# Performance work log

Measured on AMD Instinct MI355X. Metric: run time of the kernel, lower is better.

The kernel has to match this reference:

```python
import jax, jax.numpy as jnp
import numpy as np

B, N, K, NUM_CLASSES = 8, 4096, 20, 40


def _knn_idx(x, k):
    # x: [B, N, D] -> indices of k nearest neighbors (self excluded), [B, N, k]
    sq = jnp.sum(x * x, axis=-1)  # [B, N]
    dist = sq[:, :, None] + sq[:, None, :] - 2.0 * jnp.einsum('bnd,bmd->bnm', x, x)
    dist = jnp.where(jnp.eye(x.shape[1], dtype=bool)[None], jnp.inf, dist)
    return jax.lax.top_k(-dist, k)[1]


def _edge_conv(x, idx, params):
    # PyG EdgeConv with max aggregation: max_j MLP([x_i, x_j - x_i])
    x_j = jax.vmap(lambda xb, ib: xb[ib])(x, idx)              # [B, N, K, D]
    x_i = jnp.broadcast_to(x[:, :, None, :], x_j.shape)        # [B, N, K, D]
    h = jnp.concatenate([x_i, x_j - x_i], axis=-1)             # [B, N, K, 2D]
    for w, b in params:
        h = jax.nn.relu(h @ w + b)
    return jnp.max(h, axis=2)                                  # [B, N, out]


def setup_inputs() -> dict:
    key = jax.random.key(0)
    ks = jax.random.split(key, 12)

    def lin(k, i, o):  # torch Linear default init
        k1, k2 = jax.random.split(k)
        s = 1.0 / np.sqrt(i)
        return (jax.random.uniform(k1, (i, o), jnp.float32, -s, s),
                jax.random.uniform(k2, (o,), jnp.float32, -s, s))

    inp = {
        'pos': jax.random.normal(ks[0], (B * N, 3), jnp.float32),
        'batch': jnp.repeat(jnp.arange(B, dtype=jnp.int32), N),
    }
    names = [('m1w1', 'm1b1', 6, 64), ('m1w2', 'm1b2', 64, 64), ('m1w3', 'm1b3', 64, 64),
             ('m2w1', 'm2b1', 128, 128), ('m2w2', 'm2b2', 128, 128), ('m2w3', 'm2b3', 128, 256),
             ('lin0_w', 'lin0_b', 256, 512), ('lin1_w', 'lin1_b', 512, 256),
             ('lin2_w', 'lin2_b', 256, 256), ('lin3_w', 'lin3_b', 256, NUM_CLASSES)]
    for t, (wn, bn, i, o) in enumerate(names):
        w, b = lin(ks[t + 1], i, o)
        inp[wn] = w
        inp[bn] = b
    return inp


def reference(pos, batch, m1w1, m1b1, m1w2, m1b2, m1w3, m1b3,
              m2w1, m2b1, m2w2, m2b2, m2w3, m2b3,
              lin0_w, lin0_b, lin1_w, lin1_b, lin2_w, lin2_b, lin3_w, lin3_b):
    x = pos.reshape(B, N, 3)
    x = _edge_conv(x, _knn_idx(x, K), [(m1w1, m1b1), (m1w2, m1b2), (m1w3, m1b3)])   # [B,N,64]
    x = _edge_conv(x, _knn_idx(x, K), [(m2w1, m2b1), (m2w2, m2b2), (m2w3, m2b3)])   # [B,N,256]
    x = jax.nn.relu(x @ lin0_w + lin0_b)                                            # [B,N,512]
    x = jax.ops.segment_max(x.reshape(B * N, -1), batch, num_segments=B)            # [B,512]
    x = jax.nn.relu(x @ lin1_w + lin1_b)
    x = jax.nn.relu(x @ lin2_w + lin2_b)   # dropout is identity in eval mode
    x = x @ lin3_w + lin3_b
    return jax.nn.log_softmax(x, axis=-1)
```

## Files before the change

### kernel.cpp

```cpp
#include <hip/hip_runtime.h>

#define DEVI static __device__ __forceinline__

typedef __attribute__((ext_vector_type(4))) float f32x4;
typedef __attribute__((ext_vector_type(8))) short short8;
typedef __attribute__((ext_vector_type(4))) short short4v;
typedef __attribute__((ext_vector_type(8))) __bf16 bf16x8;

#define N_    4096
#define KNN_  20
#define NPTS  32768

DEVI unsigned short f2bf(float f){
  unsigned u = __float_as_uint(f);
  u += 0x7FFFu + ((u >> 16) & 1u);
  return (unsigned short)(u >> 16);
}
DEVI float bf2f(unsigned short s){ return __uint_as_float(((unsigned)s) << 16); }
DEVI float bf2fs(short s){ return __uint_as_float(((unsigned)(unsigned short)s) << 16); }
DEVI unsigned umin32(unsigned a, unsigned b){ return a < b ? a : b; }
DEVI unsigned umax32(unsigned a, unsigned b){ return a > b ? a : b; }

DEVI f32x4 mfma16(short8 a, short8 b, f32x4 c){
  return __builtin_amdgcn_mfma_f32_16x16x32_bf16(
      __builtin_bit_cast(bf16x8, a), __builtin_bit_cast(bf16x8, b), c, 0, 0, 0);
}

DEVI short8 lds_frag(const unsigned short* buf, int row, int k0, int strideS, int swzMask){
  return *(const short8*)(buf + row*strideS + (k0 ^ ((row & swzMask) << 3)));
}
DEVI void lds_put8(unsigned short* buf, int row, int k0, int strideS, int swzMask, short8 v){
  *(short8*)(buf + row*strideS + (k0 ^ ((row & swzMask) << 3))) = v;
}

DEVI void ins32(unsigned K, unsigned (&a)[20]){
#pragma unroll
  for (int t = 19; t >= 1; --t) a[t] = umin32(a[t], umax32(a[t-1], K));
  a[0] = umin32(a[0], K);
}
DEVI void ins64(double K, double (&a)[20]){
#pragma unroll
  for (int t = 19; t >= 1; --t) a[t] = fmin(a[t], fmax(a[t-1], K));
  a[0] = fmin(a[0], K);
}

__global__ __launch_bounds__(256) void p3_k(const float* __restrict__ pos,
    unsigned short* __restrict__ p3h, unsigned short* __restrict__ p3l, float* __restrict__ nrm3){
  int p = blockIdx.x*256 + threadIdx.x;
  if (p >= NPTS) return;
  float x = pos[(size_t)p*3], y = pos[(size_t)p*3+1], z = pos[(size_t)p*3+2];
  float v[8] = {x, y, z, 0.f, 0.f, 0.f, 0.f, 0.f};
#pragma unroll
  for (int c = 0; c < 8; ++c){
    unsigned short h = f2bf(v[c]);
    p3h[(size_t)p*8 + c] = h;
    p3l[(size_t)p*8 + c] = f2bf(v[c] - bf2f(h));
  }
  nrm3[p] = fmaf(x, x, fmaf(y, y, z*z));
}

template<int MODE>
__global__ __launch_bounds__(256) void knn_k(const unsigned short* __restrict__ Xh,
                                             const unsigned short* __restrict__ Xl,
                                             const float* __restrict__ nrm,
                                             unsigned* __restrict__ pk){
  constexpr int BSTR = MODE ? 4096 : 512;
  constexpr int OBL  = MODE ? 16384 : 2048;
  constexpr int OBUF = MODE ? 32768 : 4096;
  constexpr int OTHR = OBUF + 6144;
  constexpr int OSQ  = OTHR + 256;
  constexpr int SM   = MODE ? (OSQ + 512) : 15360;
  __shared__ __align__(16) char smem[SM];
  unsigned short* BhA = (unsigned short*)(smem);
  unsigned short* BlA = (unsigned short*)(smem + OBL);
  unsigned* buf      = (unsigned*)(smem + OBUF);
  unsigned* rowThr   = (unsigned*)(smem + OTHR);
  float* sqjA        = (float*)(smem + OSQ);
  unsigned* mD       = (unsigned*)(smem);

  const int blk = blockIdx.x;
  const int rt = blk & 63, ch = (blk >> 6) & 1, bb = blk >> 7;
  const int rowbase = rt * 64, cbase = ch * 2048;
  const size_t gb = (size_t)bb * N_;
  const int tid = threadIdx.x, lane = tid & 63, wid = tid >> 6;
  const int l15 = lane & 15, g = lane >> 4, kL = g << 3, r0 = g << 2;
  const int qidx = wid*16 + l15;

  if (tid < 64) rowThr[tid] = 0xFFFFFFFFu;

  short8 qh0 = {0,0,0,0,0,0,0,0}, qh1 = {0,0,0,0,0,0,0,0};
  short8 ql0 = {0,0,0,0,0,0,0,0}, ql1 = {0,0,0,0,0,0,0,0};
  if (MODE == 1){
    const size_t ab = (gb + rowbase + qidx) * 64;
    qh0 = *(const short8*)(Xh + ab + kL);
    qh1 = *(const short8*)(Xh + ab + 32 + kL);
    ql0 = *(const short8*)(Xl + ab + kL);
    ql1 = *(const short8*)(Xl + ab + 32 + kL);
  } else {
    if (g == 0){
      const size_t ab = (gb + rowbase + qidx) * 8;
      qh0 = *(const short8*)(Xh + ab);
      ql0 = *(const short8*)(Xl + ab);
    }
  }
  const float si = nrm[gb + rowbase + qidx];

  unsigned arr[20];
#pragma unroll
  for (int t = 0; t < 20; ++t) arr[t] = 0xFFFFFFFFu;
  int cnt = 0;
  bool selfR[4];
#pragma unroll
  for (int r = 0; r < 4; ++r) selfR[r] = (l15 == r0 + r);

  if (MODE == 1){
    for (int f = tid; f < 512; f += 256){
      int lf = f & 63, half = (f >> 6) & 1, ct = f >> 7;
      int row = ct*16 + (lf & 15);
      int col = half*32 + ((lf >> 4) << 3);
      const size_t src = (gb + cbase + row) * 64 + col;
      *(short8*)(BhA + f*8) = *(const short8*)(Xh + src);
      *(short8*)(BlA + f*8) = *(const short8*)(Xl + src);
    }
  } else {
    if (tid < 64)       *(short8*)(BhA + tid*8)      = *(const short8*)(Xh + (gb + cbase + tid)*8);
    else if (tid < 128) *(short8*)(BlA + (tid-64)*8) = *(const short8*)(Xl + (gb + cbase + (tid-64))*8);
  }
  if (tid < 64) sqjA[tid] = nrm[gb + cbase + tid];
  __syncthreads();

  for (int c = 0; c < 32; ++c){
    const int cur = c & 1;
    const unsigned short* Bh = BhA + cur*BSTR;
    const unsigned short* Bl = BlA + cur*BSTR;
    const float* sqj = sqjA + cur*64;
    const bool selfTile = (cbase + c*64 == rowbase);
    const bool more = (c + 1 < 32);

    short8 nh0 = {0,0,0,0,0,0,0,0}, nh1 = {0,0,0,0,0,0,0,0};
    short8 nl0 = {0,0,0,0,0,0,0,0}, nl1 = {0,0,0,0,0,0,0,0};
    float nsq = 0.f;
    if (more){
      if (MODE == 1){
#pragma unroll
        for (int ff = 0; ff < 2; ++ff){
          int f = tid + ff*256;
          int lf = f & 63, half = (f >> 6) & 1, ct = f >> 7;
          int row = ct*16 + (lf & 15);
          int col = half*32 + ((lf >> 4) << 3);
          const size_t src = (gb + cbase + (c+1)*64 + row) * 64 + col;
          if (ff == 0){ nh0 = *(const short8*)(Xh + src); nl0 = *(const short8*)(Xl + src); }
          else        { nh1 = *(const short8*)(Xh + src); nl1 = *(const short8*)(Xl + src); }
        }
      } else {
        if (tid < 64)       nh0 = *(const short8*)(Xh + (gb + cbase + (c+1)*64 + tid)*8);
        else if (tid < 128) nl0 = *(const short8*)(Xl + (gb + cbase + (c+1)*64 + (tid-64))*8);
      }
      if (tid < 64) nsq = nrm[gb + cbase + (c+1)*64 + tid];
    }

    unsigned kb16[16];
#pragma unroll
    for (int ct = 0; ct < 4; ++ct){
      f32x4 acc = {0.f,0.f,0.f,0.f};
      if (MODE == 1){
        const int fb = lane*8;
        short8 ch0 = *(const short8*)(Bh + (ct*2+0)*512 + fb);
        short8 ch1 = *(const short8*)(Bh + (ct*2+1)*512 + fb);
        short8 cl0 = *(const short8*)(Bl + (ct*2+0)*512 + fb);
        short8 cl1 = *(const short8*)(Bl + (ct*2+1)*512 + fb);
        acc = mfma16(ch0, qh0, acc); acc = mfma16(ch1, qh1, acc);
        acc = mfma16(cl0, qh0, acc); acc = mfma16(cl1, qh1, acc);
        acc = mfma16(ch0, ql0, acc); acc = mfma16(ch1, ql1, acc);
      } else {
        short8 cb = {0,0,0,0,0,0,0,0}, cl_ = {0,0,0,0,0,0,0,0};
        if (g == 0){
          cb  = *(const short8*)(Bh + (ct*16 + l15)*8);
          cl_ = *(const short8*)(Bl + (ct*16 + l15)*8);
        }
        acc = mfma16(cb,  qh0, acc);
        acc = mfma16(cl_, qh0, acc);
        acc = mfma16(cb,  ql0, acc);
      }
      f32x4 sj4 = *(const f32x4*)(sqj + ct*16 + r0);
#pragma unroll
      for (int r = 0; r < 4; ++r){
        unsigned cid = (unsigned)(c*64 + ct*16 + r0 + r);
        float dv = fmaxf(fmaf(-2.f, acc[r], si + sj4[r]), 0.f);
        unsigned kb = (__float_as_uint(dv) & ~0x7FFu) | cid;
        if (selfTile && ct == wid && selfR[r]) kb = 0x7F800000u | cid;
        kb16[ct*4 + r] = kb;
      }
    }

    {
      unsigned thrP = rowThr[qidx];
#pragma unroll
      for (int i = 0; i < 16; ++i){
        unsigned kb = kb16[i];
        if (kb < thrP){
          if (cnt < 6){ buf[cnt*256 + tid] = kb; ++cnt; }
          else ins32(kb, arr);
        }
      }
      for (int t = 0; t < cnt; ++t) ins32(buf[t*256 + tid], arr);
      cnt = 0;
      atomicMin(&rowThr[qidx], arr[19]);
    }

    if (more){
      unsigned short* BhN = BhA + (cur^1)*BSTR;
      unsigned short* BlN = BlA + (cur^1)*BSTR;
      if (MODE == 1){
        *(short8*)(BhN + tid*8)       = nh0;
        *(short8*)(BhN + (tid+256)*8) = nh1;
        *(short8*)(BlN + tid*8)       = nl0;
        *(short8*)(BlN + (tid+256)*8) = nl1;
      } else {
        if (tid < 64)       *(short8*)(BhN + tid*8)      = nh0;
        else if (tid < 128) *(short8*)(BlN + (tid-64)*8) = nl0;
      }
      if (tid < 64) sqjA[(cur^1)*64 + tid] = nsq;
    }
    __syncthreads();
  }
  __syncthreads();
  if (g > 0){
#pragma unroll
    for (int t = 0; t < 20; ++t) mD[(qidx*3 + g-1)*20 + t] = arr[t];
  }
  __syncthreads();
  if (g == 0){
    for (int gg = 0; gg < 3; ++gg)
#pragma unroll
      for (int t = 0; t < 20; ++t) ins32(mD[(qidx*3 + gg)*20 + t], arr);
    const size_t gp = gb + rowbase + qidx;
#pragma unroll
    for (int t = 0; t < 20; ++t) pk[((size_t)(ch*20 + t))*NPTS + gp] = arr[t];
  }
}

__global__ __launch_bounds__(256) void knn_merge_k(const unsigned* __restrict__ pk,
                                                   int* __restrict__ idx){
  const int p = blockIdx.x*256 + threadIdx.x;
  double arr[20];
#pragma unroll
  for (int t = 0; t < 20; ++t){
    unsigned k = pk[(size_t)t*NPTS + p];
    unsigned long long K = (((unsigned long long)(k & ~0x7FFu)) << 1) | (k & 0x7FFu);
    arr[t] = __builtin_bit_cast(double, K);
  }
#pragma unroll
  for (int t = 0; t < 20; ++t){
    unsigned k = pk[(size_t)(20 + t)*NPTS + p];
    unsigned long long K = (((unsigned long long)(k & ~0x7FFu)) << 1) | (2048u + (k & 0x7FFu));
    ins64(__builtin_bit_cast(double, K), arr);
  }
  int* o = idx + (size_t)p*KNN_;
#pragma unroll
  for (int t = 0; t < 20; ++t)
    o[t] = (int)(__builtin_bit_cast(unsigned long long, arr[t]) & 0xFFFu);
}

__global__ void stage_w_k(const float* __restrict__ src, unsigned short* __restrict__ dh,
                          unsigned short* __restrict__ dl, int K, int Nw, int KT, int NT){
  int tid = blockIdx.x*256 + threadIdx.x;
  if (tid >= NT*KT*64) return;
  int l = tid & 63;
  int kk = (tid >> 6) % KT;
  int nt = tid / (64*KT);
  int n = nt*16 + (l & 15);
  int kb = kk*32 + ((l >> 4) << 3);
#pragma unroll
  for (int e=0;e<8;++e){
    int k = kb + e;
    float w = (k < K) ? src[(size_t)k*Nw + n] : 0.f;
    unsigned short h = f2bf(w);
    dh[(size_t)tid*8 + e] = h;
    if (dl) dl[(size_t)tid*8 + e] = f2bf(w - bf2f(h));
  }
}

__global__ __launch_bounds__(256) void ec1_k(const float* __restrict__ pos, const int* __restrict__ idx1,
    const unsigned short* __restrict__ W1h, const unsigned short* __restrict__ W1l,
    const unsigned short* __restrict__ W2h, const unsigned short* __restrict__ W2l,
    const unsigned short* __restrict__ W3h, const unsigned short* __restrict__ W3l,
    const float* __restrict__ b1, const float* __restrict__ b2, const float* __restrict__ b3,
    unsigned short* __restrict__ x1h, unsigned short* __restrict__ x1l, float* __restrict__ nrm1){
  __shared__ __align__(16) char smem[51200];
  unsigned short* Ah  = (unsigned short*)(smem);
  unsigned short* Al  = (unsigned short*)(smem + 5120);
  unsigned short* H1h = (unsigned short*)(smem + 10240);
  unsigned short* H1l = (unsigned short*)(smem + 20480);
  unsigned short* H2h = (unsigned short*)(smem + 30720);
  unsigned short* H2l = (unsigned short*)(smem + 40960);
  float* dump = (float*)(smem);
  const int p0 = blockIdx.x * 4;
  const int bb = p0 >> 12;
  const int tid = threadIdx.x, lane = tid & 63, wid = tid >> 6;
  const int l15 = lane & 15, g = lane >> 4, r0 = g << 2;

  if (tid < 80){
    int p = p0 + tid/20, slot = tid%20;
    int j = idx1[(size_t)p*KNN_ + slot];
    int gj = (bb << 12) + j;
    float a6[6];
    a6[0] = pos[(size_t)p*3]; a6[1] = pos[(size_t)p*3+1]; a6[2] = pos[(size_t)p*3+2];
    a6[3] = pos[(size_t)gj*3]   - a6[0];
    a6[4] = pos[(size_t)gj*3+1] - a6[1];
    a6[5] = pos[(size_t)gj*3+2] - a6[2];
    int mt = tid >> 4, lrow = tid & 15;
    short8 vh, vl, zz = {0,0,0,0,0,0,0,0};
#pragma unroll
    for (int c=0;c<8;++c){
      float v = (c < 6) ? a6[c] : 0.f;
      unsigned short h = f2bf(v);
      vh[c] = (short)h;
      vl[c] = (short)f2bf(v - bf2f(h));
    }
    *(short8*)(Ah + (mt*64 + lrow)*8) = vh;
    *(short8*)(Al + (mt*64 + lrow)*8) = vl;
#pragma unroll
    for (int gg=1;gg<4;++gg){
      *(short8*)(Ah + (mt*64 + gg*16 + lrow)*8) = zz;
      *(short8*)(Al + (mt*64 + gg*16 + lrow)*8) = zz;
    }
  }
  __syncthreads();
  const int nt = wid;
  const int kk2 = nt >> 1, sub2 = (nt & 1)*2 + (g >> 1), e0 = (g & 1)*4;
  {
    short8 wh = *(const short8*)(W1h + ((size_t)nt*64 + lane)*8);
    short8 wl = *(const short8*)(W1l + ((size_t)nt*64 + lane)*8);
    f32x4 b4 = *(const f32x4*)(b1 + nt*16 + r0);
    for (int mt=0; mt<5; ++mt){
      short8 ah = *(const short8*)(Ah + (mt*64 + lane)*8);
      short8 al = *(const short8*)(Al + (mt*64 + lane)*8);
      f32x4 acc = {0.f,0.f,0.f,0.f};
      acc = mfma16(wh, ah, acc);
      acc = mfma16(wl, ah, acc);
      acc = mfma16(wh, al, acc);
      short4v vh4, vl4;
#pragma unroll
      for (int r=0;r<4;++r){
        float v = fmaxf(acc[r] + b4[r], 0.f);
        unsigned short h = f2bf(v);
        vh4[r] = (short)h;
        vl4[r] = (short)f2bf(v - bf2f(h));
      }
      *(short4v*)(H1h + ((mt*2 + kk2)*64 + sub2*16 + l15)*8 + e0) = vh4;
      *(short4v*)(H1l + ((mt*2 + kk2)*64 + sub2*16 + l15)*8 + e0) = vl4;
    }
  }
  __syncthreads();
  {
    short8 wh0 = *(const short8*)(W2h + ((size_t)(nt*2+0)*64 + lane)*8);
    short8 wh1 = *(const short8*)(W2h + ((size_t)(nt*2+1)*64 + lane)*8);
    short8 wl0 = *(const short8*)(W2l + ((size_t)(nt*2+0)*64 + lane)*8);
    short8 wl1 = *(const short8*)(W2l + ((size_t)(nt*2+1)*64 + lane)*8);
    f32x4 b4 = *(const f32x4*)(b2 + nt*16 + r0);
    for (int mt=0; mt<5; ++mt){
      short8 ah0 = *(const short8*)(H1h + ((mt*2+0)*64 + lane)*8);
      short8 ah1 = *(const short8*)(H1h + ((mt*2+1)*64 + lane)*8);
      short8 al0 = *(const short8*)(H1l + ((mt*2+0)*64 + lane)*8);
      short8 al1 = *(const short8*)(H1l + ((mt*2+1)*64 + lane)*8);
      f32x4 acc = {0.f,0.f,0.f,0.f};
      acc = mfma16(wh0, ah0, acc); acc = mfma16(wh1, ah1, acc);
      acc = mfma16(wl0, ah0, acc); acc = mfma16(wl1, ah1, acc);
      acc = mfma16(wh0, al0, acc); acc = mfma16(wh1, al1, acc);
      short4v vh4, vl4;
#pragma unroll
      for (int r=0;r<4;++r){
        float v = fmaxf(acc[r] + b4[r], 0.f);
        unsigned short h = f2bf(v);
        vh4[r] = (short)h;
        vl4[r] = (short)f2bf(v - bf2f(h));
      }
      *(short4v*)(H2h + ((mt*2 + kk2)*64 + sub2*16 + l15)*8 + e0) = vh4;
      *(short4v*)(H2l + ((mt*2 + kk2)*64 + sub2*16 + l15)*8 + e0) = vl4;
    }
  }
  __syncthreads();
  {
    short8 wh0 = *(const short8*)(W3h + ((size_t)(nt*2+0)*64 + lane)*8);
    short8 wh1 = *(const short8*)(W3h + ((size_t)(nt*2+1)*64 + lane)*8);
    short8 wl0 = *(const short8*)(W3l + ((size_t)(nt*2+0)*64 + lane)*8);
    short8 wl1 = *(const short8*)(W3l + ((size_t)(nt*2+1)*64 + lane)*8);
    f32x4 b4 = *(const f32x4*)(b3 + nt*16 + r0);
    for (int mt=0; mt<5; ++mt){
      short8 ah0 = *(const short8*)(H2h + ((mt*2+0)*64 + lane)*8);
      short8 ah1 = *(const short8*)(H2h + ((mt*2+1)*64 + lane)*8);
      short8 al0 = *(const short8*)(H2l + ((mt*2+0)*64 + lane)*8);
      short8 al1 = *(const short8*)(H2l + ((mt*2+1)*64 + lane)*8);
      f32x4 acc = {0.f,0.f,0.f,0.f};
      acc = mfma16(wh0, ah0, acc); acc = mfma16(wh1, ah1, acc);
      acc = mfma16(wl0, ah0, acc); acc = mfma16(wl1, ah1, acc);
      acc = mfma16(wh0, al0, acc); acc = mfma16(wh1, al1, acc);
      f32x4 o;
#pragma unroll
      for (int r=0;r<4;++r) o[r] = fmaxf(acc[r] + b4[r], 0.f);
      int edge = mt*16 + l15;
      *(f32x4*)(dump + edge*68 + nt*16 + r0) = o;
    }
  }
  __syncthreads();
  if (tid < 64){
    int p = tid >> 4, c4 = tid & 15;
    int st = tid % 20;
    float mx[4] = {0.f,0.f,0.f,0.f};
    for (int e=0;e<20;++e){
      int ee = st + e; if (ee >= 20) ee -= 20;
      f32x4 v = *(const f32x4*)(dump + (p*20 + ee)*68 + c4*4);
#pragma unroll
      for (int r=0;r<4;++r) mx[r] = fmaxf(mx[r], v[r]);
    }
    int gp = p0 + p;
    short4v h4, l4;
    float s = 0.f;
#pragma unroll
    for (int r=0;r<4;++r){
      float m = mx[r];
      unsigned short h = f2bf(m);
      h4[r] = (short)h;
      l4[r] = (short)f2bf(m - bf2f(h));
      s = fmaf(m, m, s);
    }
    *(short4v*)(x1h + (size_t)gp*64 + c4*4) = h4;
    *(short4v*)(x1l + (size_t)gp*64 + c4*4) = l4;
    s += __shfl_xor(s, 1); s += __shfl_xor(s, 2); s += __shfl_xor(s, 4); s += __shfl_xor(s, 8);
    if (c4 == 0) nrm1[gp] = s;
  }
}

__global__ __launch_bounds__(256) void ec2_k(const unsigned short* __restrict__ x1h, const int* __restrict__ idx2,
    const unsigned short* __restrict__ V1, const unsigned short* __restrict__ V2, const unsigned short* __restrict__ V3,
    const float* __restrict__ b1, const float* __restrict__ b2, const float* __restrict__ b3,
    unsigned short* __restrict__ x2b){
  __shared__ __align__(16) char smem[81920];
  unsigned short* A  = (unsigned short*)(smem);
  unsigned short* H1 = (unsigned short*)(smem + 40960);
  const int p0 = blockIdx.x * 8, bb = p0 >> 12;
  const int tid = threadIdx.x, lane = tid & 63, wid = tid >> 6;
  const int l15 = lane & 15, r0 = (lane >> 4) << 2;

  if (tid < 160){
    int p = p0 + tid/20, slot = tid%20;
    int j = idx2[(size_t)p*KNN_ + slot];
    int gj = (bb << 12) + j;
    const unsigned short* xi = x1h + (size_t)p*64;
    const unsigned short* xj = x1h + (size_t)gj*64;
    int mt = tid >> 4, lrow = tid & 15;
#pragma unroll
    for (int q=0;q<8;++q){
      short8 vi = *(const short8*)(xi + q*8);
      short8 vj = *(const short8*)(xj + q*8);
      short8 vd;
#pragma unroll
      for (int c=0;c<8;++c) vd[c] = (short)f2bf(bf2fs(vj[c]) - bf2fs(vi[c]));
      *(short8*)(A + (((mt*4 + (q>>2))*64) + (q&3)*16 + lrow)*8) = vi;
      *(short8*)(A + (((mt*4 + 2 + (q>>2))*64) + (q&3)*16 + lrow)*8) = vd;
    }
  }
  __syncthreads();

  {
    short8 w[2][4];
#pragma unroll
    for (int ni=0;ni<2;++ni)
#pragma unroll
      for (int kk=0;kk<4;++kk)
        w[ni][kk] = *(const short8*)(V1 + ((size_t)((wid*2+ni)*4+kk)*64 + lane)*8);
    f32x4 b4[2];
    b4[0] = *(const f32x4*)(b1 + (wid*2+0)*16 + r0);
    b4[1] = *(const f32x4*)(b1 + (wid*2+1)*16 + r0);
    for (int mt=0; mt<10; ++mt){
      short8 bfr[4];
#pragma unroll
      for (int kk=0;kk<4;++kk) bfr[kk] = *(const short8*)(A + ((mt*4+kk)*64 + lane)*8);
#pragma unroll
      for (int ni=0;ni<2;++ni){
        int nt = wid*2 + ni;
        f32x4 acc = {0.f,0.f,0.f,0.f};
#pragma unroll
        for (int kk=0;kk<4;++kk) acc = mfma16(w[ni][kk], bfr[kk], acc);
        short4v v4;
#pragma unroll
        for (int r=0;r<4;++r) v4[r] = (short)f2bf(fmaxf(acc[r] + b4[ni][r], 0.f));
        int kk2 = nt >> 1, sub2 = (nt & 1)*2 + (r0 >> 3);
        *(short4v*)(H1 + ((mt*4+kk2)*64 + sub2*16 + l15)*8 + (r0 & 4)) = v4;
      }
    }
  }
  __syncthreads();
  {
    short8 w[2][4];
#pragma unroll
    for (int ni=0;ni<2;++ni)
#pragma unroll
      for (int kk=0;kk<4;++kk)
        w[ni][kk] = *(const short8*)(V2 + ((size_t)((wid*2+ni)*4+kk)*64 + lane)*8);
    f32x4 b4[2];
    b4[0] = *(const f32x4*)(b2 + (wid*2+0)*16 + r0);
    b4[1] = *(const f32x4*)(b2 + (wid*2+1)*16 + r0);
    for (int mt=0; mt<10; ++mt){
      short8 bfr[4];
#pragma unroll
      for (int kk=0;kk<4;++kk) bfr[kk] = *(const short8*)(H1 + ((mt*4+kk)*64 + lane)*8);
#pragma unroll
      for (int ni=0;ni<2;++ni){
        int nt = wid*2 + ni;
        f32x4 acc = {0.f,0.f,0.f,0.f};
#pragma unroll
        for (int kk=0;kk<4;++kk) acc = mfma16(w[ni][kk], bfr[kk], acc);
        short4v v4;
#pragma unroll
        for (int r=0;r<4;++r) v4[r] = (short)f2bf(fmaxf(acc[r] + b4[ni][r], 0.f));
        int kk2 = nt >> 1, sub2 = (nt & 1)*2 + (r0 >> 3);
        *(short4v*)(A + ((mt*4+kk2)*64 + sub2*16 + l15)*8 + (r0 & 4)) = v4;
      }
    }
  }
  __syncthreads();
  for (int g2=0; g2<2; ++g2){
    {
      short8 w[2][4];
#pragma unroll
      for (int ni=0;ni<2;++ni)
#pragma unroll
        for (int kk=0;kk<4;++kk)
          w[ni][kk] = *(const short8*)(V3 + ((size_t)((g2*8 + wid*2+ni)*4+kk)*64 + lane)*8);
      f32x4 b4[2];
      b4[0] = *(const f32x4*)(b3 + (g2*8 + wid*2+0)*16 + r0);
      b4[1] = *(const f32x4*)(b3 + (g2*8 + wid*2+1)*16 + r0);
      for (int mt=0; mt<10; ++mt){
        short8 bfr[4];
#pragma unroll
        for (int kk=0;kk<4;++kk) bfr[kk] = *(const short8*)(A + ((mt*4+kk)*64 + lane)*8);
#pragma unroll
        for (int ni=0;ni<2;++ni){
          int ntl = wid*2 + ni;
          f32x4 acc = {0.f,0.f,0.f,0.f};
#pragma unroll
          for (int kk=0;kk<4;++kk) acc = mfma16(w[ni][kk], bfr[kk], acc);
          short4v v4;
#pragma unroll
          for (int r=0;r<4;++r) v4[r] = (short)f2bf(fmaxf(acc[r] + b4[ni][r], 0.f));
          int kk2 = ntl >> 1, sub2 = (ntl & 1)*2 + (r0 >> 3);
          *(short4v*)(H1 + ((mt*4+kk2)*64 + sub2*16 + l15)*8 + (r0 & 4)) = v4;
        }
      }
    }
    __syncthreads();
    if (tid < 128){
      int p = tid >> 4, c8 = tid & 15;
      int kk = c8 >> 2, sub = c8 & 3;
      unsigned short mx[8];
#pragma unroll
      for (int e=0;e<8;++e) mx[e] = 0;
      for (int e=0;e<20;++e){
        int ee = e + p + c8; ee -= (ee >= 20) ? 20 : 0; ee -= (ee >= 20) ? 20 : 0;
        int row = p*20 + ee;
        short8 v = *(const short8*)(H1 + (((row>>4)*4 + kk)*64 + sub*16 + (row & 15))*8);
#pragma unroll
        for (int k2=0;k2<8;++k2){
          unsigned short u = (unsigned short)v[k2];
          mx[k2] = u > mx[k2] ? u : mx[k2];
        }
      }
      short8 o;
#pragma unroll
      for (int k2=0;k2<8;++k2) o[k2] = (short)mx[k2];
      *(short8*)(x2b + (size_t)(p0 + p)*256 + g2*128 + c8*8) = o;
    }
    __syncthreads();
  }
}

__global__ __launch_bounds__(256) void lin0_k(const unsigned short* __restrict__ x2b, const unsigned short* __restrict__ W0s,
                                              const float* __restrict__ b0, unsigned* __restrict__ pool){
  __shared__ __align__(16) char smem[67584];
  unsigned short* A = (unsigned short*)(smem);
  unsigned* ploc = (unsigned*)(smem + 65536);
  const int blk = blockIdx.x; const size_t row0 = (size_t)blk * 128; const int bb = blk >> 5;
  const int tid = threadIdx.x, lane = tid & 63, wid = tid >> 6;
  for (int it = tid; it < 4096; it += 256){
    int row = it >> 5, q = (it & 31) << 3;
    lds_put8(A, row, q, 256, 7, *(const short8*)(x2b + (row0 + row)*256 + q));
  }
  ploc[tid] = 0u; ploc[tid+256] = 0u;
  __syncthreads();
  const int l15 = lane & 15, kL = (lane >> 4) << 3;
  short8 af[2][8];
#pragma unroll
  for (int m=0;m<2;++m)
#pragma unroll
    for (int kk=0;kk<8;++kk)
      af[m][kk] = lds_frag(A, (wid*2+m)*16 + l15, kk*32 + kL, 256, 7);
  for (int nt=0; nt<32; ++nt){
    f32x4 a0 = {0.f,0.f,0.f,0.f}, a1 = {0.f,0.f,0.f,0.f};
#pragma unroll
    for (int kk=0;kk<8;++kk){
      short8 w = *(const short8*)(W0s + ((size_t)(nt*8+kk)*64 + lane)*8);
      a0 = mfma16(af[0][kk], w, a0);
      a1 = mfma16(af[1][kk], w, a1);
    }
    int col = nt*16 + l15;
    float m = fmaxf(fmaxf(fmaxf(a0[0],a0[1]),fmaxf(a0[2],a0[3])),
                    fmaxf(fmaxf(a1[0],a1[1]),fmaxf(a1[2],a1[3])));
    m = fmaxf(m + b0[col], 0.f);
    atomicMax(&ploc[col], __float_as_uint(m));
  }
  __syncthreads();
  atomicMax(&pool[(size_t)bb*512 + tid], ploc[tid]);
  atomicMax(&pool[(size_t)bb*512 + tid + 256], ploc[tid+256]);
}

__global__ __launch_bounds__(256) void head_k(const unsigned* __restrict__ pool,
    const float* __restrict__ w1, const float* __restrict__ bb1,
    const float* __restrict__ w2, const float* __restrict__ bb2,
    const float* __restrict__ w3, const float* __restrict__ bb3,
    float* __restrict__ out){
  __shared__ float pl[8*512];
  __shared__ float y1[8*256];
  __shared__ float y2[8*256];
  __shared__ float lg[8*40];
  const int tid = threadIdx.x;
  for (int it = tid; it < 4096; it += 256) pl[it] = __uint_as_float(pool[it]);
  __syncthreads();
  {
    float acc[8]; float bv = bb1[tid];
#pragma unroll
    for (int r=0;r<8;++r) acc[r] = bv;
    for (int k=0;k<512;++k){
      float w = w1[(size_t)k*256 + tid];
#pragma unroll
      for (int r=0;r<8;++r) acc[r] = fmaf(pl[r*512+k], w, acc[r]);
    }
#pragma unroll
    for (int r=0;r<8;++r) y1[r*256+tid] = fmaxf(acc[r], 0.f);
  }
  __syncthreads();
  {
    float acc[8]; float bv = bb2[tid];
#pragma unroll
    for (int r=0;r<8;++r) acc[r] = bv;
    for (int k=0;k<256;++k){
      float w = w2[(size_t)k*256 + tid];
#pragma unroll
      for (int r=0;r<8;++r) acc[r] = fmaf(y1[r*256+k], w, acc[r]);
    }
#pragma unroll
    for (int r=0;r<8;++r) y2[r*256+tid] = fmaxf(acc[r], 0.f);
  }
  __syncthreads();
  if (tid < 40){
    float acc[8]; float bv = bb3[tid];
#pragma unroll
    for (int r=0;r<8;++r) acc[r] = bv;
    for (int k=0;k<256;++k){
      float w = w3[(size_t)k*40 + tid];
#pragma unroll
      for (int r=0;r<8;++r) acc[r] = fmaf(y2[r*256+k], w, acc[r]);
    }
#pragma unroll
    for (int r=0;r<8;++r) lg[r*40+tid] = acc[r];
  }
  __syncthreads();
  if (tid < 8){
    float m = -__builtin_inff();
    for (int c2=0;c2<40;++c2) m = fmaxf(m, lg[tid*40+c2]);
    float s = 0.f;
    for (int c2=0;c2<40;++c2) s += expf(lg[tid*40+c2] - m);
    float L = logf(s);
    for (int c2=0;c2<40;++c2) out[tid*40+c2] = lg[tid*40+c2] - m - L;
  }
}

extern "C" void kernel_launch(void* const* d_in, const int* in_sizes, int n_in,
                              void* d_out, int out_size, void* d_ws, size_t ws_size,
                              hipStream_t stream){
  (void)in_sizes; (void)n_in; (void)out_size; (void)ws_size;
  const float* pos  = (const float*)d_in[0];
  const float* m1w1 = (const float*)d_in[2];  const float* m1b1 = (const float*)d_in[3];
  const float* m1w2 = (const float*)d_in[4];  const float* m1b2 = (const float*)d_in[5];
  const float* m1w3 = (const float*)d_in[6];  const float* m1b3 = (const float*)d_in[7];
  const float* m2w1 = (const float*)d_in[8];  const float* m2b1 = (const float*)d_in[9];
  const float* m2w2 = (const float*)d_in[10]; const float* m2b2 = (const float*)d_in[11];
  const float* m2w3 = (const float*)d_in[12]; const float* m2b3 = (const float*)d_in[13];
  const float* l0w  = (const float*)d_in[14]; const float* l0b  = (const float*)d_in[15];
  const float* l1w  = (const float*)d_in[16]; const float* l1b  = (const float*)d_in[17];
  const float* l2w  = (const float*)d_in[18]; const float* l2b  = (const float*)d_in[19];
  const float* l3w  = (const float*)d_in[20]; const float* l3b  = (const float*)d_in[21];

  char* ws = (char*)d_ws;
  size_t o = 0;
  auto alloc = [&](size_t bytes){ size_t r = o; o += (bytes + 255) & ~(size_t)255; return r; };
  size_t o_idx1 = alloc((size_t)NPTS*20*4);
  size_t o_idx2 = alloc((size_t)NPTS*20*4);
  size_t o_x1h  = alloc((size_t)NPTS*64*2);
  size_t o_x1l  = alloc((size_t)NPTS*64*2);
  size_t o_nrm  = alloc((size_t)NPTS*4);
  size_t o_x2b  = alloc((size_t)NPTS*256*2);
  size_t o_pool = alloc(8*512*4);
  size_t o_p3h  = alloc((size_t)NPTS*8*2);
  size_t o_p3l  = alloc((size_t)NPTS*8*2);
  size_t o_nrm3 = alloc((size_t)NPTS*4);
  size_t o_pk   = alloc((size_t)2*20*NPTS*4);
  size_t o_W1h = alloc(4*1*64*8*2),  o_W1l = alloc(4*1*64*8*2);
  size_t o_W2h = alloc(4*2*64*8*2),  o_W2l = alloc(4*2*64*8*2);
  size_t o_W3h = alloc(4*2*64*8*2),  o_W3l = alloc(4*2*64*8*2);
  size_t o_V1  = alloc(8*4*64*8*2);
  size_t o_V2  = alloc(8*4*64*8*2);
  size_t o_V3  = alloc(16*4*64*8*2);
  size_t o_W0  = alloc(32*8*64*8*2);

  hipMemsetAsync(ws + o_pool, 0, 8*512*4, stream);

  stage_w_k<<<1,256,0,stream>>>(m1w1, (unsigned short*)(ws+o_W1h), (unsigned short*)(ws+o_W1l), 6, 64, 1, 4);
  stage_w_k<<<2,256,0,stream>>>(m1w2, (unsigned short*)(ws+o_W2h), (unsigned short*)(ws+o_W2l), 64, 64, 2, 4);
  stage_w_k<<<2,256,0,stream>>>(m1w3, (unsigned short*)(ws+o_W3h), (unsigned short*)(ws+o_W3l), 64, 64, 2, 4);
  stage_w_k<<<8,256,0,stream>>>(m2w1, (unsigned short*)(ws+o_V1), nullptr, 128, 128, 4, 8);
  stage_w_k<<<8,256,0,stream>>>(m2w2, (unsigned short*)(ws+o_V2), nullptr, 128, 128, 4, 8);
  stage_w_k<<<16,256,0,stream>>>(m2w3, (unsigned short*)(ws+o_V3), nullptr, 128, 256, 4, 16);
  stage_w_k<<<64,256,0,stream>>>(l0w,  (unsigned short*)(ws+o_W0), nullptr, 256, 512, 8, 32);

  p3_k<<<128,256,0,stream>>>(pos, (unsigned short*)(ws+o_p3h), (unsigned short*)(ws+o_p3l), (float*)(ws+o_nrm3));

  knn_k<0><<<1024,256,0,stream>>>((const unsigned short*)(ws+o_p3h), (const unsigned short*)(ws+o_p3l),
                                  (const float*)(ws+o_nrm3), (unsigned*)(ws+o_pk));
  knn_merge_k<<<128,256,0,stream>>>((const unsigned*)(ws+o_pk), (int*)(ws+o_idx1));

  ec1_k<<<8192,256,0,stream>>>(pos, (const int*)(ws+o_idx1),
      (const unsigned short*)(ws+o_W1h), (const unsigned short*)(ws+o_W1l),
      (const unsigned short*)(ws+o_W2h), (const unsigned short*)(ws+o_W2l),
      (const unsigned short*)(ws+o_W3h), (const unsigned short*)(ws+o_W3l),
      m1b1, m1b2, m1b3,
      (unsigned short*)(ws+o_x1h), (unsigned short*)(ws+o_x1l), (float*)(ws+o_nrm));

  knn_k<1><<<1024,256,0,stream>>>((const unsigned short*)(ws+o_x1h), (const unsigned short*)(ws+o_x1l),
                                  (const float*)(ws+o_nrm), (unsigned*)(ws+o_pk));
  knn_merge_k<<<128,256,0,stream>>>((const unsigned*)(ws+o_pk), (int*)(ws+o_idx2));

  ec2_k<<<4096,256,0,stream>>>((const unsigned short*)(ws+o_x1h), (const int*)(ws+o_idx2),
      (const unsigned short*)(ws+o_V1), (const unsigned short*)(ws+o_V2), (const unsigned short*)(ws+o_V3),
      m2b1, m2b2, m2b3, (unsigned short*)(ws+o_x2b));

  lin0_k<<<256,256,0,stream>>>((const unsigned short*)(ws+o_x2b), (const unsigned short*)(ws+o_W0),
                               l0b, (unsigned*)(ws+o_pool));

  head_k<<<1,256,0,stream>>>((const unsigned*)(ws+o_pool), l1w, l1b, l2w, l2b, l3w, l3b, (float*)d_out);
}
```

Before: 656.3 us.

## Merge staging kernels, drop LDS tiling in kNN, split head per batch

Fuses the point-conversion kernel and seven weight-staging launches into one kernel to cut launch overhead. The kNN kernel stops double-buffering candidate tiles through shared memory and reads MFMA fragments and norms straight from global memory, removing a per-tile barrier. The classifier head now runs one block per batch row instead of a single block. The kNN change adds redundant global/L2 loads across waves in exchange for less synchronisation and lower LDS usage.

```diff
diff --git a/kernel.cpp b/kernel.cpp
--- a/kernel.cpp
+++ b/kernel.cpp
@@ -44,19 +44,56 @@
   a[0] = fmin(a[0], K);
 }
 
-__global__ __launch_bounds__(256) void p3_k(const float* __restrict__ pos,
-    unsigned short* __restrict__ p3h, unsigned short* __restrict__ p3l, float* __restrict__ nrm3){
-  int p = blockIdx.x*256 + threadIdx.x;
-  if (p >= NPTS) return;
-  float x = pos[(size_t)p*3], y = pos[(size_t)p*3+1], z = pos[(size_t)p*3+2];
-  float v[8] = {x, y, z, 0.f, 0.f, 0.f, 0.f, 0.f};
-#pragma unroll
-  for (int c = 0; c < 8; ++c){
-    unsigned short h = f2bf(v[c]);
-    p3h[(size_t)p*8 + c] = h;
-    p3l[(size_t)p*8 + c] = f2bf(v[c] - bf2f(h));
-  }
-  nrm3[p] = fmaf(x, x, fmaf(y, y, z*z));
+DEVI void stage_body(const float* __restrict__ src, unsigned short* __restrict__ dh,
+                     unsigned short* __restrict__ dl, int K, int Nw, int KT, int lblk){
+  int tid = lblk*256 + (int)threadIdx.x;
+  int l = tid & 63;
+  int kk = (tid >> 6) % KT;
+  int nt = tid / (64*KT);
+  int n = nt*16 + (l & 15);
+  int kb = kk*32 + ((l >> 4) << 3);
+#pragma unroll
+  for (int e=0;e<8;++e){
+    int k = kb + e;
+    float w = (k < K) ? src[(size_t)k*Nw + n] : 0.f;
+    unsigned short h = f2bf(w);
+    dh[(size_t)tid*8 + e] = h;
+    if (dl) dl[(size_t)tid*8 + e] = f2bf(w - bf2f(h));
+  }
+}
+
+__global__ __launch_bounds__(256) void stage_all_k(const float* __restrict__ pos,
+    unsigned short* __restrict__ p3h, unsigned short* __restrict__ p3l, float* __restrict__ nrm3,
+    const float* __restrict__ m1w1, const float* __restrict__ m1w2, const float* __restrict__ m1w3,
+    const float* __restrict__ m2w1, const float* __restrict__ m2w2, const float* __restrict__ m2w3,
+    const float* __restrict__ l0w,
+    unsigned short* __restrict__ W1h, unsigned short* __restrict__ W1l,
+    unsigned short* __restrict__ W2h, unsigned short* __restrict__ W2l,
+    unsigned short* __restrict__ W3h, unsigned short* __restrict__ W3l,
+    unsigned short* __restrict__ V1, unsigned short* __restrict__ V2, unsigned short* __restrict__ V3,
+    unsigned short* __restrict__ W0){
+  const int blk = blockIdx.x;
+  if (blk < 128){
+    int p = blk*256 + (int)threadIdx.x;
+    float x = pos[(size_t)p*3], y = pos[(size_t)p*3+1], z = pos[(size_t)p*3+2];
+    float v[8] = {x, y, z, 0.f, 0.f, 0.f, 0.f, 0.f};
+#pragma unroll
+    for (int c = 0; c < 8; ++c){
+      unsigned short h = f2bf(v[c]);
+      p3h[(size_t)p*8 + c] = h;
+      p3l[(size_t)p*8 + c] = f2bf(v[c] - bf2f(h));
+    }
+    nrm3[p] = fmaf(x, x, fmaf(y, y, z*z));
+    return;
+  }
+  int b = blk - 128;
+  if      (b < 1)  stage_body(m1w1, W1h, W1l, 6,   64,  1, b);
+  else if (b < 3)  stage_body(m1w2, W2h, W2l, 64,  64,  2, b-1);
+  else if (b < 5)  stage_body(m1w3, W3h, W3l, 64,  64,  2, b-3);
+  else if (b < 13) stage_body(m2w1, V1, nullptr, 128, 128, 4, b-5);
+  else if (b < 21) stage_body(m2w2, V2, nullptr, 128, 128, 4, b-13);
+  else if (b < 37) stage_body(m2w3, V3, nullptr, 128, 256, 4, b-21);
+  else             stage_body(l0w,  W0, nullptr, 256, 512, 8, b-37);
 }
 
 template<int MODE>
@@ -64,19 +101,10 @@
                                              const unsigned short* __restrict__ Xl,
                                              const float* __restrict__ nrm,
                                              unsigned* __restrict__ pk){
-  constexpr int BSTR = MODE ? 4096 : 512;
-  constexpr int OBL  = MODE ? 16384 : 2048;
-  constexpr int OBUF = MODE ? 32768 : 4096;
-  constexpr int OTHR = OBUF + 6144;
-  constexpr int OSQ  = OTHR + 256;
-  constexpr int SM   = MODE ? (OSQ + 512) : 15360;
-  __shared__ __align__(16) char smem[SM];
-  unsigned short* BhA = (unsigned short*)(smem);
-  unsigned short* BlA = (unsigned short*)(smem + OBL);
-  unsigned* buf      = (unsigned*)(smem + OBUF);
-  unsigned* rowThr   = (unsigned*)(smem + OTHR);
-  float* sqjA        = (float*)(smem + OSQ);
-  unsigned* mD       = (unsigned*)(smem);
+  __shared__ __align__(16) char smem[15616];
+  unsigned* buf    = (unsigned*)(smem);
+  unsigned* rowThr = (unsigned*)(smem + 6144);
+  unsigned* mD     = (unsigned*)(smem);
 
   const int blk = blockIdx.x;
   const int rt = blk & 63, ch = (blk >> 6) & 1, bb = blk >> 7;
@@ -113,76 +141,35 @@
 #pragma unroll
   for (int r = 0; r < 4; ++r) selfR[r] = (l15 == r0 + r);
 
-  if (MODE == 1){
-    for (int f = tid; f < 512; f += 256){
-      int lf = f & 63, half = (f >> 6) & 1, ct = f >> 7;
-      int row = ct*16 + (lf & 15);
-      int col = half*32 + ((lf >> 4) << 3);
-      const size_t src = (gb + cbase + row) * 64 + col;
-      *(short8*)(BhA + f*8) = *(const short8*)(Xh + src);
-      *(short8*)(BlA + f*8) = *(const short8*)(Xl + src);
-    }
-  } else {
-    if (tid < 64)       *(short8*)(BhA + tid*8)      = *(const short8*)(Xh + (gb + cbase + tid)*8);
-    else if (tid < 128) *(short8*)(BlA + (tid-64)*8) = *(const short8*)(Xl + (gb + cbase + (tid-64))*8);
-  }
-  if (tid < 64) sqjA[tid] = nrm[gb + cbase + tid];
   __syncthreads();
 
   for (int c = 0; c < 32; ++c){
-    const int cur = c & 1;
-    const unsigned short* Bh = BhA + cur*BSTR;
-    const unsigned short* Bl = BlA + cur*BSTR;
-    const float* sqj = sqjA + cur*64;
     const bool selfTile = (cbase + c*64 == rowbase);
-    const bool more = (c + 1 < 32);
-
-    short8 nh0 = {0,0,0,0,0,0,0,0}, nh1 = {0,0,0,0,0,0,0,0};
-    short8 nl0 = {0,0,0,0,0,0,0,0}, nl1 = {0,0,0,0,0,0,0,0};
-    float nsq = 0.f;
-    if (more){
-      if (MODE == 1){
-#pragma unroll
-        for (int ff = 0; ff < 2; ++ff){
-          int f = tid + ff*256;
-          int lf = f & 63, half = (f >> 6) & 1, ct = f >> 7;
-          int row = ct*16 + (lf & 15);
-          int col = half*32 + ((lf >> 4) << 3);
-          const size_t src = (gb + cbase + (c+1)*64 + row) * 64 + col;
-          if (ff == 0){ nh0 = *(const short8*)(Xh + src); nl0 = *(const short8*)(Xl + src); }
-          else        { nh1 = *(const short8*)(Xh + src); nl1 = *(const short8*)(Xl + src); }
-        }
-      } else {
-        if (tid < 64)       nh0 = *(const short8*)(Xh + (gb + cbase + (c+1)*64 + tid)*8);
-        else if (tid < 128) nl0 = *(const short8*)(Xl + (gb + cbase + (c+1)*64 + (tid-64))*8);
-      }
-      if (tid < 64) nsq = nrm[gb + cbase + (c+1)*64 + tid];
-    }
-
     unsigned kb16[16];
 #pragma unroll
     for (int ct = 0; ct < 4; ++ct){
       f32x4 acc = {0.f,0.f,0.f,0.f};
       if (MODE == 1){
-        const int fb = lane*8;
-        short8 ch0 = *(const short8*)(Bh + (ct*2+0)*512 + fb);
-        short8 ch1 = *(const short8*)(Bh + (ct*2+1)*512 + fb);
-        short8 cl0 = *(const short8*)(Bl + (ct*2+0)*512 + fb);
-        short8 cl1 = *(const short8*)(Bl + (ct*2+1)*512 + fb);
+        const size_t cb64 = (gb + cbase + c*64 + ct*16 + l15) * 64;
+        short8 ch0 = *(const short8*)(Xh + cb64 + kL);
+        short8 ch1 = *(const short8*)(Xh + cb64 + 32 + kL);
+        short8 cl0 = *(const short8*)(Xl + cb64 + kL);
+        short8 cl1 = *(const short8*)(Xl + cb64 + 32 + kL);
         acc = mfma16(ch0, qh0, acc); acc = mfma16(ch1, qh1, acc);
         acc = mfma16(cl0, qh0, acc); acc = mfma16(cl1, qh1, acc);
         acc = mfma16(ch0, ql0, acc); acc = mfma16(ch1, ql1, acc);
       } else {
         short8 cb = {0,0,0,0,0,0,0,0}, cl_ = {0,0,0,0,0,0,0,0};
         if (g == 0){
-          cb  = *(const short8*)(Bh + (ct*16 + l15)*8);
-          cl_ = *(const short8*)(Bl + (ct*16 + l15)*8);
+          const size_t cb8 = (size_t)(gb + cbase + c*64 + ct*16 + l15) * 8;
+          cb  = *(const short8*)(Xh + cb8);
+          cl_ = *(const short8*)(Xl + cb8);
         }
         acc = mfma16(cb,  qh0, acc);
         acc = mfma16(cl_, qh0, acc);
         acc = mfma16(cb,  ql0, acc);
       }
-      f32x4 sj4 = *(const f32x4*)(sqj + ct*16 + r0);
+      f32x4 sj4 = *(const f32x4*)(nrm + gb + cbase + c*64 + ct*16 + r0);
 #pragma unroll
       for (int r = 0; r < 4; ++r){
         unsigned cid = (unsigned)(c*64 + ct*16 + r0 + r);
@@ -192,7 +179,6 @@
         kb16[ct*4 + r] = kb;
       }
     }
-
     {
       unsigned thrP = rowThr[qidx];
 #pragma unroll
@@ -207,22 +193,6 @@
       cnt = 0;
       atomicMin(&rowThr[qidx], arr[19]);
     }
-
-    if (more){
-      unsigned short* BhN = BhA + (cur^1)*BSTR;
-      unsigned short* BlN = BlA + (cur^1)*BSTR;
-      if (MODE == 1){
-        *(short8*)(BhN + tid*8)       = nh0;
-        *(short8*)(BhN + (tid+256)*8) = nh1;
-        *(short8*)(BlN + tid*8)       = nl0;
-        *(short8*)(BlN + (tid+256)*8) = nl1;
-      } else {
-        if (tid < 64)       *(short8*)(BhN + tid*8)      = nh0;
-        else if (tid < 128) *(short8*)(BlN + (tid-64)*8) = nl0;
-      }
-      if (tid < 64) sqjA[(cur^1)*64 + tid] = nsq;
-    }
-    __syncthreads();
   }
   __syncthreads();
   if (g > 0){
@@ -260,25 +230,6 @@
 #pragma unroll
   for (int t = 0; t < 20; ++t)
     o[t] = (int)(__builtin_bit_cast(unsigned long long, arr[t]) & 0xFFFu);
-}
-
-__global__ void stage_w_k(const float* __restrict__ src, unsigned short* __restrict__ dh,
-                          unsigned short* __restrict__ dl, int K, int Nw, int KT, int NT){
-  int tid = blockIdx.x*256 + threadIdx.x;
-  if (tid >= NT*KT*64) return;
-  int l = tid & 63;
-  int kk = (tid >> 6) % KT;
-  int nt = tid / (64*KT);
-  int n = nt*16 + (l & 15);
-  int kb = kk*32 + ((l >> 4) << 3);
-#pragma unroll
-  for (int e=0;e<8;++e){
-    int k = kb + e;
-    float w = (k < K) ? src[(size_t)k*Nw + n] : 0.f;
-    unsigned short h = f2bf(w);
-    dh[(size_t)tid*8 + e] = h;
-    if (dl) dl[(size_t)tid*8 + e] = f2bf(w - bf2f(h));
-  }
 }
 
 __global__ __launch_bounds__(256) void ec1_k(const float* __restrict__ pos, const int* __restrict__ idx1,
@@ -615,64 +566,43 @@
   atomicMax(&pool[(size_t)bb*512 + tid + 256], ploc[tid+256]);
 }
 
-__global__ __launch_bounds__(256) void head_k(const unsigned* __restrict__ pool,
+__global__ __launch_bounds__(256) void head8_k(const unsigned* __restrict__ pool,
     const float* __restrict__ w1, const float* __restrict__ bb1,
     const float* __restrict__ w2, const float* __restrict__ bb2,
     const float* __restrict__ w3, const float* __restrict__ bb3,
     float* __restrict__ out){
-  __shared__ float pl[8*512];
-  __shared__ float y1[8*256];
-  __shared__ float y2[8*256];
-  __shared__ float lg[8*40];
+  __shared__ float pl[512];
+  __shared__ float y1[256];
+  __shared__ float y2[256];
+  __shared__ float lg[40];
+  const int row = blockIdx.x;
   const int tid = threadIdx.x;
-  for (int it = tid; it < 4096; it += 256) pl[it] = __uint_as_float(pool[it]);
+  for (int it = tid; it < 512; it += 256) pl[it] = __uint_as_float(pool[row*512 + it]);
   __syncthreads();
   {
-    float acc[8]; float bv = bb1[tid];
-#pragma unroll
-    for (int r=0;r<8;++r) acc[r] = bv;
-    for (int k=0;k<512;++k){
-      float w = w1[(size_t)k*256 + tid];
-#pragma unroll
-      for (int r=0;r<8;++r) acc[r] = fmaf(pl[r*512+k], w, acc[r]);
-    }
-#pragma unroll
-    for (int r=0;r<8;++r) y1[r*256+tid] = fmaxf(acc[r], 0.f);
+    float acc = bb1[tid];
+    for (int k=0;k<512;++k) acc = fmaf(pl[k], w1[(size_t)k*256 + tid], acc);
+    y1[tid] = fmaxf(acc, 0.f);
   }
   __syncthreads();
   {
-    float acc[8]; float bv = bb2[tid];
-#pragma unroll
-    for (int r=0;r<8;++r) acc[r] = bv;
-    for (int k=0;k<256;++k){
-      float w = w2[(size_t)k*256 + tid];
-#pragma unroll
-      for (int r=0;r<8;++r) acc[r] = fmaf(y1[r*256+k], w, acc[r]);
-    }
-#pragma unroll
-    for (int r=0;r<8;++r) y2[r*256+tid] = fmaxf(acc[r], 0.f);
+    float acc = bb2[tid];
+    for (int k=0;k<256;++k) acc = fmaf(y1[k], w2[(size_t)k*256 + tid], acc);
+    y2[tid] = fmaxf(acc, 0.f);
   }
   __syncthreads();
   if (tid < 40){
-    float acc[8]; float bv = bb3[tid];
-#pragma unroll
-    for (int r=0;r<8;++r) acc[r] = bv;
-    for (int k=0;k<256;++k){
-      float w = w3[(size_t)k*40 + tid];
-#pragma unroll
-      for (int r=0;r<8;++r) acc[r] = fmaf(y2[r*256+k], w, acc[r]);
-    }
-#pragma unroll
-    for (int r=0;r<8;++r) lg[r*40+tid] = acc[r];
-  }
-  __syncthreads();
-  if (tid < 8){
+    float acc = bb3[tid];
+    for (int k=0;k<256;++k) acc = fmaf(y2[k], w3[(size_t)k*40 + tid], acc);
+    lg[tid] = acc;
+  }
+  __syncthreads();
+  if (tid < 40){
     float m = -__builtin_inff();
-    for (int c2=0;c2<40;++c2) m = fmaxf(m, lg[tid*40+c2]);
+    for (int c2=0;c2<40;++c2) m = fmaxf(m, lg[c2]);
     float s = 0.f;
-    for (int c2=0;c2<40;++c2) s += expf(lg[tid*40+c2] - m);
-    float L = logf(s);
-    for (int c2=0;c2<40;++c2) out[tid*40+c2] = lg[tid*40+c2] - m - L;
+    for (int c2=0;c2<40;++c2) s += expf(lg[c2] - m);
+    out[row*40 + tid] = lg[tid] - m - logf(s);
   }
 }
 
@@ -716,15 +646,14 @@
 
   hipMemsetAsync(ws + o_pool, 0, 8*512*4, stream);
 
-  stage_w_k<<<1,256,0,stream>>>(m1w1, (unsigned short*)(ws+o_W1h), (unsigned short*)(ws+o_W1l), 6, 64, 1, 4);
-  stage_w_k<<<2,256,0,stream>>>(m1w2, (unsigned short*)(ws+o_W2h), (unsigned short*)(ws+o_W2l), 64, 64, 2, 4);
-  stage_w_k<<<2,256,0,stream>>>(m1w3, (unsigned short*)(ws+o_W3h), (unsigned short*)(ws+o_W3l), 64, 64, 2, 4);
-  stage_w_k<<<8,256,0,stream>>>(m2w1, (unsigned short*)(ws+o_V1), nullptr, 128, 128, 4, 8);
-  stage_w_k<<<8,256,0,stream>>>(m2w2, (unsigned short*)(ws+o_V2), nullptr, 128, 128, 4, 8);
-  stage_w_k<<<16,256,0,stream>>>(m2w3, (unsigned short*)(ws+o_V3), nullptr, 128, 256, 4, 16);
-  stage_w_k<<<64,256,0,stream>>>(l0w,  (unsigned short*)(ws+o_W0), nullptr, 256, 512, 8, 32);
-
-  p3_k<<<128,256,0,stream>>>(pos, (unsigned short*)(ws+o_p3h), (unsigned short*)(ws+o_p3l), (float*)(ws+o_nrm3));
+  stage_all_k<<<229,256,0,stream>>>(pos,
+      (unsigned short*)(ws+o_p3h), (unsigned short*)(ws+o_p3l), (float*)(ws+o_nrm3),
+      m1w1, m1w2, m1w3, m2w1, m2w2, m2w3, l0w,
+      (unsigned short*)(ws+o_W1h), (unsigned short*)(ws+o_W1l),
+      (unsigned short*)(ws+o_W2h), (unsigned short*)(ws+o_W2l),
+      (unsigned short*)(ws+o_W3h), (unsigned short*)(ws+o_W3l),
+      (unsigned short*)(ws+o_V1), (unsigned short*)(ws+o_V2), (unsigned short*)(ws+o_V3),
+      (unsigned short*)(ws+o_W0));
 
   knn_k<0><<<1024,256,0,stream>>>((const unsigned short*)(ws+o_p3h), (const unsigned short*)(ws+o_p3l),
                                   (const float*)(ws+o_nrm3), (unsigned*)(ws+o_pk));
@@ -748,5 +677,5 @@
   lin0_k<<<256,256,0,stream>>>((const unsigned short*)(ws+o_x2b), (const unsigned short*)(ws+o_W0),
                                l0b, (unsigned*)(ws+o_pool));
 
-  head_k<<<1,256,0,stream>>>((const unsigned*)(ws+o_pool), l1w, l1b, l2w, l2b, l3w, l3b, (float*)d_out);
-}
+  head8_k<<<8,256,0,stream>>>((const unsigned*)(ws+o_pool), l1w, l1b, l2w, l2b, l3w, l3b, (float*)d_out);
+}
```

Result: slower. 691.5 us (+5.4%).
